# Performance work log

Hardware: AMD Instinct MI355X
Metric: run time of the kernel (lower is better)

Reference implementation:

```python
import jax, jax.numpy as jnp
import numpy as np

# geomloss SamplesLoss(loss='sinkhorn', p=2, reach=1.0, blur=0.1) constants
P = 2
BLUR = 0.1
REACH = 1.0
SCALING = 0.5
EPS_FINAL = BLUR ** P          # 0.01
RHO = REACH ** P               # 1.0
DIAMETER = 2.0 * np.sqrt(2.0)  # PMT positions scaled to [-1,1]^2


def eps_schedule():
    # geomloss epsilon_schedule(p, diameter, blur, scaling)
    e = [DIAMETER ** P]
    for t in np.arange(P * np.log(DIAMETER), P * np.log(BLUR), P * np.log(SCALING)):
        e.append(float(np.exp(t)))
    e.append(BLUR ** P)
    return [float(v) for v in e]


def _softmin(eps, C, h):
    # h: (B, N) log-measure + potential/eps ; C: (N, N) shared cost -> (B, N)
    return -eps * jax.scipy.special.logsumexp(h[:, None, :] - C[None, :, :] / eps, axis=-1)


def _sinkhorn_potentials(a_log, b_log, C):
    # symmetric unbalanced Sinkhorn loop with eps-annealing (geomloss sinkhorn_loop)
    eps_list = eps_schedule()
    damp = lambda eps: 1.0 / (1.0 + eps / RHO)
    eps0 = eps_list[0]
    d0 = damp(eps0)
    g_ab = d0 * _softmin(eps0, C, a_log)
    f_ba = d0 * _softmin(eps0, C, b_log)
    f_aa = d0 * _softmin(eps0, C, a_log)
    g_bb = d0 * _softmin(eps0, C, b_log)
    for eps in eps_list:
        d = damp(eps)
        ft = d * _softmin(eps, C, b_log + g_ab / eps)
        gt = d * _softmin(eps, C, a_log + f_ba / eps)
        f_ba, g_ab = 0.5 * (f_ba + ft), 0.5 * (g_ab + gt)
        f_aa = 0.5 * (f_aa + d * _softmin(eps, C, a_log + f_aa / eps))
        g_bb = 0.5 * (g_bb + d * _softmin(eps, C, b_log + g_bb / eps))
    # last extrapolation at the final (target) temperature
    eps = eps_list[-1]
    d = damp(eps)
    f_ba, g_ab = (d * _softmin(eps, C, b_log + g_ab / eps),
                  d * _softmin(eps, C, a_log + f_ba / eps))
    f_aa = d * _softmin(eps, C, a_log + f_aa / eps)
    g_bb = d * _softmin(eps, C, b_log + g_bb / eps)
    return f_aa, g_bb, g_ab, f_ba


def setup_inputs() -> dict:
    key = jax.random.key(0)
    k1, k2, k3 = jax.random.split(key, 3)
    B, N = 32768, 32
    # positive PE weights (measure masses must be > 0 for log-domain Sinkhorn)
    pred_pmtpe = jax.random.uniform(k1, (B, N), jnp.float32, 0.05, 1.0)
    target_pe = jax.random.uniform(k2, (B, N), jnp.float32, 0.05, 1.0)
    # fixed scaled 2D (z,y) PMT layout in [-1,1]^2, shared by pred and target clouds
    pmt_pos = jax.random.uniform(k3, (N, 2), jnp.float32, -1.0, 1.0)
    batchstart = jnp.arange(B, dtype=jnp.int64) * N
    batchend = batchstart + N
    return {"pred_pmtpe": pred_pmtpe, "target_pe": target_pe, "pmt_pos": pmt_pos,
            "batchstart": batchstart, "batchend": batchend}


def reference(pred_pmtpe, target_pe, pmt_pos, batchstart, batchend):
    # shared cost matrix (x_pred_batch == y_target_batch == PMT layout), C = |x-y|^2/2 for p=2
    C = 0.5 * jnp.sum((pmt_pos[:, None, :] - pmt_pos[None, :, :]) ** 2, axis=-1)  # (32,32)
    # geomloss runs the Sinkhorn loop with autograd disabled (envelope theorem)
    a_log = jnp.log(jax.lax.stop_gradient(pred_pmtpe))
    b_log = jnp.log(jax.lax.stop_gradient(target_pe))
    f_aa, g_bb, g_ab, f_ba = _sinkhorn_potentials(a_log, b_log, C)
    f_aa, g_bb, g_ab, f_ba = map(jax.lax.stop_gradient, (f_aa, g_bb, g_ab, f_ba))
    # unbalanced debiased sinkhorn cost (geomloss sinkhorn_cost, rho finite)
    eps = EPS_FINAL
    scale = RHO + 0.5 * eps
    per_batch = scale * (
        jnp.sum(pred_pmtpe * (jnp.exp(-f_aa / RHO) - jnp.exp(-f_ba / RHO)), axis=-1)
        + jnp.sum(target_pe * (jnp.exp(-g_bb / RHO) - jnp.exp(-g_ab / RHO)), axis=-1)
    )
    return jnp.mean(per_batch)
```

## Files before the change

kernel.cpp:

```cpp
#include <hip/hip_runtime.h>

#define EXP2F(x)  __builtin_amdgcn_exp2f(x)
#define LOG2FD(x) __builtin_amdgcn_logf(x)
#define L2E 1.4426950408889634f
#define T1F 1.2621774e-29f

typedef __attribute__((ext_vector_type(8))) short bf16x8;
typedef __attribute__((ext_vector_type(4))) float f32x4;

#define MFMA16(A, B, C) __builtin_amdgcn_mfma_f32_16x16x32_bf16((A), (B), (C), 0, 0, 0)

union U8 { unsigned int u[4]; bf16x8 v; };

__device__ __forceinline__ void split_pack(const float* w, bf16x8& hi, bf16x8& lo) {
  U8 a, b;
#pragma unroll
  for (int k = 0; k < 4; ++k) {
    float x0 = w[2*k], x1 = w[2*k+1];
    unsigned u0 = __float_as_uint(x0) & 0xFFFF0000u;
    unsigned u1 = __float_as_uint(x1) & 0xFFFF0000u;
    float r0 = x0 - __uint_as_float(u0);
    float r1 = x1 - __uint_as_float(u1);
    a.u[k] = (u0 >> 16) | u1;
    b.u[k] = ((__float_as_uint(r0) & 0xFFFF0000u) >> 16) |
             (__float_as_uint(r1) & 0xFFFF0000u);
  }
  hi = a.v; lo = b.v;
}

struct P1 {
  bf16x8 KA1, KA2, KB1, KB2;
  float Gab[8], Fba[8], Faa[8], Gbb[8];
  float al2[8], bl2[8];
};

__device__ __forceinline__ void buildK(const float* c2a, const float* c2b, float inv,
                                       bf16x8& KA1, bf16x8& KA2, bf16x8& KB1, bf16x8& KB2) {
  float ka[8], kb[8];
#pragma unroll
  for (int e = 0; e < 8; ++e) { ka[e] = EXP2F(-c2a[e] * inv); kb[e] = EXP2F(-c2b[e] * inv); }
  split_pack(ka, KA1, KA2);
  split_pack(kb, KB1, KB2);
}

__device__ __forceinline__ void pot_assign(float* pot, const float* Ts, int b15, int g) {
  float4 r0 = *(const float4*)&Ts[b15*36 + 8*g];
  float4 r1 = *(const float4*)&Ts[b15*36 + 8*g + 4];
  pot[0]=r0.x; pot[1]=r0.y; pot[2]=r0.z; pot[3]=r0.w;
  pot[4]=r1.x; pot[5]=r1.y; pot[6]=r1.z; pot[7]=r1.w;
}

__device__ __forceinline__ void pot_merge(float* pot, const float* Ts, int b15, int g) {
  float4 r0 = *(const float4*)&Ts[b15*36 + 8*g];
  float4 r1 = *(const float4*)&Ts[b15*36 + 8*g + 4];
  pot[0]=0.5f*(pot[0]+r0.x); pot[1]=0.5f*(pot[1]+r0.y);
  pot[2]=0.5f*(pot[2]+r0.z); pot[3]=0.5f*(pot[3]+r0.w);
  pot[4]=0.5f*(pot[4]+r1.x); pot[5]=0.5f*(pot[5]+r1.y);
  pot[6]=0.5f*(pot[6]+r1.z); pot[7]=0.5f*(pot[7]+r1.w);
}

__device__ __noinline__ float exact_lse(const float2* pos2, const float* HB,
                                        int i, float inv) {
  float2 pi = pos2[i];
  float m = -3.4e38f;
#pragma unroll 1
  for (int j = 0; j < 32; ++j) {
    float2 pj = pos2[j];
    float dx = pi.x - pj.x, dy = pi.y - pj.y;
    float arg = fmaf((0.5f*L2E)*(dx*dx + dy*dy), -inv, HB[j]);
    m = fmaxf(m, arg);
  }
  float s = 0.f;
#pragma unroll 1
  for (int j = 0; j < 32; ++j) {
    float2 pj = pos2[j];
    float dx = pi.x - pj.x, dy = pi.y - pj.y;
    float arg = fmaf((0.5f*L2E)*(dx*dx + dy*dy), -inv, HB[j]);
    s += EXP2F(arg - m);
  }
  return m + LOG2FD(s);
}

template<bool CHECKED>
__device__ __forceinline__ void ksoft(float* Ts, float* Hdump, const float* H,
    bf16x8 KA1, bf16x8 KA2, bf16x8 KB1, bf16x8 KB2,
    float nde, float inv, int b15, int g, const float2* pos2) {
  float hm = fmaxf(fmaxf(fmaxf(H[0], H[1]), fmaxf(H[2], H[3])),
                   fmaxf(fmaxf(H[4], H[5]), fmaxf(H[6], H[7])));
  hm = fmaxf(hm, __shfl_xor(hm, 16));
  hm = fmaxf(hm, __shfl_xor(hm, 32));
  float d[8], w[8];
#pragma unroll
  for (int e = 0; e < 8; ++e) { d[e] = H[e] - hm; w[e] = EXP2F(d[e]); }
  bf16x8 w1, w2;
  split_pack(w, w1, w2);
  f32x4 z = {0.f, 0.f, 0.f, 0.f};
  f32x4 a0 = MFMA16(KA1, w1, z);
  a0 = MFMA16(KA2, w1, a0);
  a0 = MFMA16(KA1, w2, a0);
  f32x4 a1 = MFMA16(KB1, w1, z);
  a1 = MFMA16(KB2, w1, a1);
  a1 = MFMA16(KB1, w2, a1);
  float r0[4], r1[4];
#pragma unroll
  for (int r = 0; r < 4; ++r) {
    r0[r] = hm + LOG2FD(a0[r]);
    r1[r] = hm + LOG2FD(a1[r]);
  }
  if (CHECKED) {
    float mn = fminf(fminf(fminf(a0[0], a0[1]), fminf(a0[2], a0[3])),
                     fminf(fminf(a1[0], a1[1]), fminf(a1[2], a1[3])));
    if (__any(mn < T1F)) {
      float wb[8];
#pragma unroll
      for (int e = 0; e < 8; ++e) wb[e] = EXP2F(d[e] + 96.f);
      bf16x8 u1, u2;
      split_pack(wb, u1, u2);
      f32x4 b0 = MFMA16(KA1, u1, z);
      b0 = MFMA16(KA2, u1, b0);
      b0 = MFMA16(KA1, u2, b0);
      f32x4 b1 = MFMA16(KB1, u1, z);
      b1 = MFMA16(KB2, u1, b1);
      b1 = MFMA16(KB1, u2, b1);
      bool mybad = false;
#pragma unroll
      for (int r = 0; r < 4; ++r) {
        if (a0[r] < T1F) r0[r] = (hm - 96.f) + LOG2FD(b0[r]);
        if (a1[r] < T1F) r1[r] = (hm - 96.f) + LOG2FD(b1[r]);
        mybad |= (a0[r] < T1F) && (b0[r] < T1F);
        mybad |= (a1[r] < T1F) && (b1[r] < T1F);
      }
      if (__any(mybad)) {
        float4 h0 = {H[0], H[1], H[2], H[3]};
        float4 h1 = {H[4], H[5], H[6], H[7]};
        *(float4*)&Hdump[b15*36 + 8*g]     = h0;
        *(float4*)&Hdump[b15*36 + 8*g + 4] = h1;
        asm volatile("" ::: "memory");
        const float* HB = &Hdump[b15*36];
#pragma unroll
        for (int r = 0; r < 4; ++r) {
          if ((a0[r] < T1F) && (b0[r] < T1F)) r0[r] = exact_lse(pos2, HB, 4*g + r, inv);
          if ((a1[r] < T1F) && (b1[r] < T1F)) r1[r] = exact_lse(pos2, HB, 16 + 4*g + r, inv);
        }
      }
    }
  }
  float4 v0 = {nde*r0[0], nde*r0[1], nde*r0[2], nde*r0[3]};
  float4 v1 = {nde*r1[0], nde*r1[1], nde*r1[2], nde*r1[3]};
  *(float4*)&Ts[b15*36 + 4*g]      = v0;
  *(float4*)&Ts[b15*36 + 4*g + 16] = v1;
}

template<bool CHECKED>
__device__ __forceinline__ void p_iter(P1& s, float* Tw, float* Hdump,
    float inv, float nde, bool mergeFirst, int b15, int g, const float2* pos2) {
  if (mergeFirst) {
    pot_merge(s.Fba, Tw + 0*576, b15, g);
    pot_merge(s.Gab, Tw + 1*576, b15, g);
    pot_merge(s.Faa, Tw + 2*576, b15, g);
    pot_merge(s.Gbb, Tw + 3*576, b15, g);
  }
  float H[8];
#pragma unroll
  for (int e = 0; e < 8; ++e) H[e] = fmaf(s.Gab[e], inv, s.bl2[e]);
  ksoft<CHECKED>(Tw + 0*576, Hdump, H, s.KA1, s.KA2, s.KB1, s.KB2, nde, inv, b15, g, pos2);
#pragma unroll
  for (int e = 0; e < 8; ++e) H[e] = fmaf(s.Fba[e], inv, s.al2[e]);
  ksoft<CHECKED>(Tw + 1*576, Hdump, H, s.KA1, s.KA2, s.KB1, s.KB2, nde, inv, b15, g, pos2);
#pragma unroll
  for (int e = 0; e < 8; ++e) H[e] = fmaf(s.Faa[e], inv, s.al2[e]);
  ksoft<CHECKED>(Tw + 2*576, Hdump, H, s.KA1, s.KA2, s.KB1, s.KB2, nde, inv, b15, g, pos2);
#pragma unroll
  for (int e = 0; e < 8; ++e) H[e] = fmaf(s.Gbb[e], inv, s.bl2[e]);
  ksoft<CHECKED>(Tw + 3*576, Hdump, H, s.KA1, s.KA2, s.KB1, s.KB2, nde, inv, b15, g, pos2);
}

__global__ __launch_bounds__(64, 2) void sink_kernel(
    const float* __restrict__ pred, const float* __restrict__ tgt,
    const float* __restrict__ pos, float* __restrict__ ws) {
  __shared__ __align__(16) float sT[4][576];
  __shared__ __align__(16) float sHb[16][36];

  const int lid = threadIdx.x;
  const int b15 = lid & 15;
  const int g   = lid >> 4;
  const int bbase = blockIdx.x * 16;
  const float2* pos2 = (const float2*)pos;
  float* Tw = &sT[0][0];
  float* Hd = &sHb[0][0];

  P1 s;
  {
    const float* pr = &pred[(bbase + b15) * 32 + 8 * g];
    const float* tr = &tgt [(bbase + b15) * 32 + 8 * g];
    float4 p0 = *(const float4*)&pr[0];
    float4 p1 = *(const float4*)&pr[4];
    float4 t0 = *(const float4*)&tr[0];
    float4 t1 = *(const float4*)&tr[4];
    s.al2[0]=LOG2FD(p0.x); s.al2[1]=LOG2FD(p0.y); s.al2[2]=LOG2FD(p0.z); s.al2[3]=LOG2FD(p0.w);
    s.al2[4]=LOG2FD(p1.x); s.al2[5]=LOG2FD(p1.y); s.al2[6]=LOG2FD(p1.z); s.al2[7]=LOG2FD(p1.w);
    s.bl2[0]=LOG2FD(t0.x); s.bl2[1]=LOG2FD(t0.y); s.bl2[2]=LOG2FD(t0.z); s.bl2[3]=LOG2FD(t0.w);
    s.bl2[4]=LOG2FD(t1.x); s.bl2[5]=LOG2FD(t1.y); s.bl2[6]=LOG2FD(t1.z); s.bl2[7]=LOG2FD(t1.w);
  }
  float c2a[8], c2b[8];
  {
    float2 pm0 = pos2[b15];
    float2 pm1 = pos2[b15 + 16];
#pragma unroll
    for (int e = 0; e < 8; ++e) {
      float2 pj = pos2[8*g + e];
      float dx0 = pm0.x - pj.x, dy0 = pm0.y - pj.y;
      float dx1 = pm1.x - pj.x, dy1 = pm1.y - pj.y;
      c2a[e] = (0.5f*L2E)*(dx0*dx0 + dy0*dy0);
      c2b[e] = (0.5f*L2E)*(dx1*dx1 + dy1*dy1);
    }
  }

  buildK(c2a, c2b, 0.125f, s.KA1, s.KA2, s.KB1, s.KB2);
  ksoft<false>(Tw + 1*576, Hd, s.al2, s.KA1, s.KA2, s.KB1, s.KB2, -8.f/9.f, 0.125f, b15, g, pos2);
  ksoft<false>(Tw + 0*576, Hd, s.bl2, s.KA1, s.KA2, s.KB1, s.KB2, -8.f/9.f, 0.125f, b15, g, pos2);
  pot_assign(s.Gab, Tw + 1*576, b15, g);
  pot_assign(s.Fba, Tw + 0*576, b15, g);
#pragma unroll
  for (int e = 0; e < 8; ++e) { s.Faa[e] = s.Gab[e]; s.Gbb[e] = s.Fba[e]; }

  p_iter<false>(s, Tw, Hd, 0.125f, -8.f/9.f, false, b15, g, pos2);
  p_iter<false>(s, Tw, Hd, 0.125f, -8.f/9.f, true,  b15, g, pos2);
  buildK(c2a, c2b, 0.5f, s.KA1, s.KA2, s.KB1, s.KB2);
  p_iter<false>(s, Tw, Hd, 0.5f, -2.f/3.f, true, b15, g, pos2);
  buildK(c2a, c2b, 2.f, s.KA1, s.KA2, s.KB1, s.KB2);
  p_iter<false>(s, Tw, Hd, 2.f, -1.f/3.f, true, b15, g, pos2);
  buildK(c2a, c2b, 8.f, s.KA1, s.KA2, s.KB1, s.KB2);
  p_iter<false>(s, Tw, Hd, 8.f, -1.f/9.f, true, b15, g, pos2);
  buildK(c2a, c2b, 32.f, s.KA1, s.KA2, s.KB1, s.KB2);
  p_iter<true>(s, Tw, Hd, 32.f, -1.f/33.f, true, b15, g, pos2);
  buildK(c2a, c2b, 100.f, s.KA1, s.KA2, s.KB1, s.KB2);
  p_iter<true>(s, Tw, Hd, 100.f, -1.f/101.f, true, b15, g, pos2);

  pot_merge(s.Fba, Tw + 0*576, b15, g);
  pot_merge(s.Gab, Tw + 1*576, b15, g);
  pot_merge(s.Faa, Tw + 2*576, b15, g);
  pot_merge(s.Gbb, Tw + 3*576, b15, g);
  {
    float H[8];
#pragma unroll
    for (int e = 0; e < 8; ++e) H[e] = fmaf(s.Gab[e], 100.f, s.bl2[e]);
    ksoft<true>(Tw + 0*576, Hd, H, s.KA1, s.KA2, s.KB1, s.KB2, -1.f/101.f, 100.f, b15, g, pos2);
#pragma unroll
    for (int e = 0; e < 8; ++e) H[e] = fmaf(s.Fba[e], 100.f, s.al2[e]);
    ksoft<true>(Tw + 1*576, Hd, H, s.KA1, s.KA2, s.KB1, s.KB2, -1.f/101.f, 100.f, b15, g, pos2);
#pragma unroll
    for (int e = 0; e < 8; ++e) H[e] = fmaf(s.Faa[e], 100.f, s.al2[e]);
    ksoft<true>(Tw + 2*576, Hd, H, s.KA1, s.KA2, s.KB1, s.KB2, -1.f/101.f, 100.f, b15, g, pos2);
#pragma unroll
    for (int e = 0; e < 8; ++e) H[e] = fmaf(s.Gbb[e], 100.f, s.bl2[e]);
    ksoft<true>(Tw + 3*576, Hd, H, s.KA1, s.KA2, s.KB1, s.KB2, -1.f/101.f, 100.f, b15, g, pos2);
  }
  pot_assign(s.Fba, Tw + 0*576, b15, g);
  pot_assign(s.Gab, Tw + 1*576, b15, g);
  pot_assign(s.Faa, Tw + 2*576, b15, g);
  pot_assign(s.Gbb, Tw + 3*576, b15, g);

  float c = 0.f;
#pragma unroll
  for (int e = 0; e < 8; ++e) {
    c += EXP2F(s.al2[e]) * (EXP2F(-s.Faa[e]) - EXP2F(-s.Fba[e]))
       + EXP2F(s.bl2[e]) * (EXP2F(-s.Gbb[e]) - EXP2F(-s.Gab[e]));
  }
  c += __shfl_xor(c, 1);
  c += __shfl_xor(c, 2);
  c += __shfl_xor(c, 4);
  c += __shfl_xor(c, 8);
  c += __shfl_xor(c, 16);
  c += __shfl_xor(c, 32);
  if (lid == 0) ws[blockIdx.x] = c;
}

__global__ __launch_bounds__(256) void reduce_kernel(
    const float* __restrict__ ws, float* __restrict__ out, int n, float scale) {
  float s = 0.f;
  for (int i = threadIdx.x; i < n; i += 256) s += ws[i];
  s += __shfl_xor(s, 32);
  s += __shfl_xor(s, 16);
  s += __shfl_xor(s, 8);
  s += __shfl_xor(s, 4);
  s += __shfl_xor(s, 2);
  s += __shfl_xor(s, 1);
  __shared__ float a[4];
  if ((threadIdx.x & 63) == 0) a[threadIdx.x >> 6] = s;
  __syncthreads();
  if (threadIdx.x == 0) out[0] = ((a[0] + a[1]) + (a[2] + a[3])) * scale;
}

extern "C" void kernel_launch(void* const* d_in, const int* in_sizes, int n_in,
                              void* d_out, int out_size, void* d_ws, size_t ws_size,
                              hipStream_t stream) {
  const float* pred = (const float*)d_in[0];
  const float* tgt  = (const float*)d_in[1];
  const float* pos  = (const float*)d_in[2];
  const int B = in_sizes[0] / 32;
  const int nblocks = B / 16;
  float* ws = (float*)d_ws;

  sink_kernel<<<nblocks, 64, 0, stream>>>(pred, tgt, pos, ws);
  reduce_kernel<<<1, 256, 0, stream>>>(ws, (float*)d_out, nblocks,
                                       1.005f / (float)B);
}
```

Before: 30.33 us.

## Split cross and self Sinkhorn chains across two wavefronts per block

Each block now runs two wavefronts. Wave 0 handles the cross potentials (f_ba, g_ab) and wave 1 handles the self potentials (f_aa, g_bb), so each wave runs two softmin calls per iteration instead of four. This roughly halves the serial dependency chain per wave and doubles the number of wavefronts in flight. In exchange it duplicates the K construction and log loads in both waves, adds __syncthreads per iteration, and writes twice as many partial sums for the reduction.

```diff
diff --git a/kernel.cpp b/kernel.cpp
--- a/kernel.cpp
+++ b/kernel.cpp
@@ -27,12 +27,6 @@
   }
   hi = a.v; lo = b.v;
 }
-
-struct P1 {
-  bf16x8 KA1, KA2, KB1, KB2;
-  float Gab[8], Fba[8], Faa[8], Gbb[8];
-  float al2[8], bl2[8];
-};
 
 __device__ __forceinline__ void buildK(const float* c2a, const float* c2b, float inv,
                                        bf16x8& KA1, bf16x8& KA2, bf16x8& KB1, bf16x8& KB2) {
@@ -152,44 +146,40 @@
 }
 
 template<bool CHECKED>
-__device__ __forceinline__ void p_iter(P1& s, float* Tw, float* Hdump,
-    float inv, float nde, bool mergeFirst, int b15, int g, const float2* pos2) {
-  if (mergeFirst) {
-    pot_merge(s.Fba, Tw + 0*576, b15, g);
-    pot_merge(s.Gab, Tw + 1*576, b15, g);
-    pot_merge(s.Faa, Tw + 2*576, b15, g);
-    pot_merge(s.Gbb, Tw + 3*576, b15, g);
-  }
-  float H[8];
-#pragma unroll
-  for (int e = 0; e < 8; ++e) H[e] = fmaf(s.Gab[e], inv, s.bl2[e]);
-  ksoft<CHECKED>(Tw + 0*576, Hdump, H, s.KA1, s.KA2, s.KB1, s.KB2, nde, inv, b15, g, pos2);
-#pragma unroll
-  for (int e = 0; e < 8; ++e) H[e] = fmaf(s.Fba[e], inv, s.al2[e]);
-  ksoft<CHECKED>(Tw + 1*576, Hdump, H, s.KA1, s.KA2, s.KB1, s.KB2, nde, inv, b15, g, pos2);
-#pragma unroll
-  for (int e = 0; e < 8; ++e) H[e] = fmaf(s.Faa[e], inv, s.al2[e]);
-  ksoft<CHECKED>(Tw + 2*576, Hdump, H, s.KA1, s.KA2, s.KB1, s.KB2, nde, inv, b15, g, pos2);
-#pragma unroll
-  for (int e = 0; e < 8; ++e) H[e] = fmaf(s.Gbb[e], inv, s.bl2[e]);
-  ksoft<CHECKED>(Tw + 3*576, Hdump, H, s.KA1, s.KA2, s.KB1, s.KB2, nde, inv, b15, g, pos2);
-}
-
-__global__ __launch_bounds__(64, 2) void sink_kernel(
+__device__ __forceinline__ void chain_iter(bool cross, float* X, float* Y,
+    const float* al2, const float* bl2, float* TX, float* TY, float* Hd,
+    bf16x8 KA1, bf16x8 KA2, bf16x8 KB1, bf16x8 KB2,
+    float inv, float nde, bool avg, int b15, int g, const float2* pos2) {
+  float HX[8], HY[8];
+#pragma unroll
+  for (int e = 0; e < 8; ++e) {
+    float xin = cross ? Y[e] : X[e];
+    float yin = cross ? X[e] : Y[e];
+    HX[e] = fmaf(xin, inv, bl2[e]);
+    HY[e] = fmaf(yin, inv, al2[e]);
+  }
+  ksoft<CHECKED>(TX, Hd, HX, KA1, KA2, KB1, KB2, nde, inv, b15, g, pos2);
+  ksoft<CHECKED>(TY, Hd, HY, KA1, KA2, KB1, KB2, nde, inv, b15, g, pos2);
+  __syncthreads();
+  if (avg) { pot_merge(X, TX, b15, g);  pot_merge(Y, TY, b15, g); }
+  else     { pot_assign(X, TX, b15, g); pot_assign(Y, TY, b15, g); }
+}
+
+__global__ __launch_bounds__(128, 4) void sink_kernel(
     const float* __restrict__ pred, const float* __restrict__ tgt,
     const float* __restrict__ pos, float* __restrict__ ws) {
-  __shared__ __align__(16) float sT[4][576];
-  __shared__ __align__(16) float sHb[16][36];
-
-  const int lid = threadIdx.x;
+  __shared__ __align__(16) float sT[2][2][576];
+  __shared__ __align__(16) float sHb[2][16][36];
+
+  const int lid = threadIdx.x & 63;
+  const int wid = threadIdx.x >> 6;
+  const bool cross = (wid == 0);
   const int b15 = lid & 15;
   const int g   = lid >> 4;
   const int bbase = blockIdx.x * 16;
   const float2* pos2 = (const float2*)pos;
-  float* Tw = &sT[0][0];
-  float* Hd = &sHb[0][0];
-
-  P1 s;
+
+  float al2[8], bl2[8];
   {
     const float* pr = &pred[(bbase + b15) * 32 + 8 * g];
     const float* tr = &tgt [(bbase + b15) * 32 + 8 * g];
@@ -197,10 +187,10 @@
     float4 p1 = *(const float4*)&pr[4];
     float4 t0 = *(const float4*)&tr[0];
     float4 t1 = *(const float4*)&tr[4];
-    s.al2[0]=LOG2FD(p0.x); s.al2[1]=LOG2FD(p0.y); s.al2[2]=LOG2FD(p0.z); s.al2[3]=LOG2FD(p0.w);
-    s.al2[4]=LOG2FD(p1.x); s.al2[5]=LOG2FD(p1.y); s.al2[6]=LOG2FD(p1.z); s.al2[7]=LOG2FD(p1.w);
-    s.bl2[0]=LOG2FD(t0.x); s.bl2[1]=LOG2FD(t0.y); s.bl2[2]=LOG2FD(t0.z); s.bl2[3]=LOG2FD(t0.w);
-    s.bl2[4]=LOG2FD(t1.x); s.bl2[5]=LOG2FD(t1.y); s.bl2[6]=LOG2FD(t1.z); s.bl2[7]=LOG2FD(t1.w);
+    al2[0]=LOG2FD(p0.x); al2[1]=LOG2FD(p0.y); al2[2]=LOG2FD(p0.z); al2[3]=LOG2FD(p0.w);
+    al2[4]=LOG2FD(p1.x); al2[5]=LOG2FD(p1.y); al2[6]=LOG2FD(p1.z); al2[7]=LOG2FD(p1.w);
+    bl2[0]=LOG2FD(t0.x); bl2[1]=LOG2FD(t0.y); bl2[2]=LOG2FD(t0.z); bl2[3]=LOG2FD(t0.w);
+    bl2[4]=LOG2FD(t1.x); bl2[5]=LOG2FD(t1.y); bl2[6]=LOG2FD(t1.z); bl2[7]=LOG2FD(t1.w);
   }
   float c2a[8], c2b[8];
   {
@@ -216,64 +206,59 @@
     }
   }
 
-  buildK(c2a, c2b, 0.125f, s.KA1, s.KA2, s.KB1, s.KB2);
-  ksoft<false>(Tw + 1*576, Hd, s.al2, s.KA1, s.KA2, s.KB1, s.KB2, -8.f/9.f, 0.125f, b15, g, pos2);
-  ksoft<false>(Tw + 0*576, Hd, s.bl2, s.KA1, s.KA2, s.KB1, s.KB2, -8.f/9.f, 0.125f, b15, g, pos2);
-  pot_assign(s.Gab, Tw + 1*576, b15, g);
-  pot_assign(s.Fba, Tw + 0*576, b15, g);
-#pragma unroll
-  for (int e = 0; e < 8; ++e) { s.Faa[e] = s.Gab[e]; s.Gbb[e] = s.Fba[e]; }
-
-  p_iter<false>(s, Tw, Hd, 0.125f, -8.f/9.f, false, b15, g, pos2);
-  p_iter<false>(s, Tw, Hd, 0.125f, -8.f/9.f, true,  b15, g, pos2);
-  buildK(c2a, c2b, 0.5f, s.KA1, s.KA2, s.KB1, s.KB2);
-  p_iter<false>(s, Tw, Hd, 0.5f, -2.f/3.f, true, b15, g, pos2);
-  buildK(c2a, c2b, 2.f, s.KA1, s.KA2, s.KB1, s.KB2);
-  p_iter<false>(s, Tw, Hd, 2.f, -1.f/3.f, true, b15, g, pos2);
-  buildK(c2a, c2b, 8.f, s.KA1, s.KA2, s.KB1, s.KB2);
-  p_iter<false>(s, Tw, Hd, 8.f, -1.f/9.f, true, b15, g, pos2);
-  buildK(c2a, c2b, 32.f, s.KA1, s.KA2, s.KB1, s.KB2);
-  p_iter<true>(s, Tw, Hd, 32.f, -1.f/33.f, true, b15, g, pos2);
-  buildK(c2a, c2b, 100.f, s.KA1, s.KA2, s.KB1, s.KB2);
-  p_iter<true>(s, Tw, Hd, 100.f, -1.f/101.f, true, b15, g, pos2);
-
-  pot_merge(s.Fba, Tw + 0*576, b15, g);
-  pot_merge(s.Gab, Tw + 1*576, b15, g);
-  pot_merge(s.Faa, Tw + 2*576, b15, g);
-  pot_merge(s.Gbb, Tw + 3*576, b15, g);
-  {
-    float H[8];
-#pragma unroll
-    for (int e = 0; e < 8; ++e) H[e] = fmaf(s.Gab[e], 100.f, s.bl2[e]);
-    ksoft<true>(Tw + 0*576, Hd, H, s.KA1, s.KA2, s.KB1, s.KB2, -1.f/101.f, 100.f, b15, g, pos2);
-#pragma unroll
-    for (int e = 0; e < 8; ++e) H[e] = fmaf(s.Fba[e], 100.f, s.al2[e]);
-    ksoft<true>(Tw + 1*576, Hd, H, s.KA1, s.KA2, s.KB1, s.KB2, -1.f/101.f, 100.f, b15, g, pos2);
-#pragma unroll
-    for (int e = 0; e < 8; ++e) H[e] = fmaf(s.Faa[e], 100.f, s.al2[e]);
-    ksoft<true>(Tw + 2*576, Hd, H, s.KA1, s.KA2, s.KB1, s.KB2, -1.f/101.f, 100.f, b15, g, pos2);
-#pragma unroll
-    for (int e = 0; e < 8; ++e) H[e] = fmaf(s.Gbb[e], 100.f, s.bl2[e]);
-    ksoft<true>(Tw + 3*576, Hd, H, s.KA1, s.KA2, s.KB1, s.KB2, -1.f/101.f, 100.f, b15, g, pos2);
-  }
-  pot_assign(s.Fba, Tw + 0*576, b15, g);
-  pot_assign(s.Gab, Tw + 1*576, b15, g);
-  pot_assign(s.Faa, Tw + 2*576, b15, g);
-  pot_assign(s.Gbb, Tw + 3*576, b15, g);
-
-  float c = 0.f;
+  float* TX = &sT[wid][0][0];
+  float* TY = &sT[wid][1][0];
+  float* Hd = &sHb[wid][0][0];
+
+  bf16x8 KA1, KA2, KB1, KB2;
+  float X[8], Y[8];
+
+  buildK(c2a, c2b, 0.125f, KA1, KA2, KB1, KB2);
+  ksoft<false>(TX, Hd, bl2, KA1, KA2, KB1, KB2, -8.f/9.f, 0.125f, b15, g, pos2);
+  ksoft<false>(TY, Hd, al2, KA1, KA2, KB1, KB2, -8.f/9.f, 0.125f, b15, g, pos2);
+  __syncthreads();
+  pot_assign(X, TX, b15, g);
+  pot_assign(Y, TY, b15, g);
+
+  chain_iter<false>(cross, X, Y, al2, bl2, TX, TY, Hd, KA1,KA2,KB1,KB2,
+                    0.125f, -8.f/9.f, true, b15, g, pos2);
+  chain_iter<false>(cross, X, Y, al2, bl2, TX, TY, Hd, KA1,KA2,KB1,KB2,
+                    0.125f, -8.f/9.f, true, b15, g, pos2);
+  buildK(c2a, c2b, 0.5f, KA1, KA2, KB1, KB2);
+  chain_iter<false>(cross, X, Y, al2, bl2, TX, TY, Hd, KA1,KA2,KB1,KB2,
+                    0.5f, -2.f/3.f, true, b15, g, pos2);
+  buildK(c2a, c2b, 2.f, KA1, KA2, KB1, KB2);
+  chain_iter<false>(cross, X, Y, al2, bl2, TX, TY, Hd, KA1,KA2,KB1,KB2,
+                    2.f, -1.f/3.f, true, b15, g, pos2);
+  buildK(c2a, c2b, 8.f, KA1, KA2, KB1, KB2);
+  chain_iter<false>(cross, X, Y, al2, bl2, TX, TY, Hd, KA1,KA2,KB1,KB2,
+                    8.f, -1.f/9.f, true, b15, g, pos2);
+  buildK(c2a, c2b, 32.f, KA1, KA2, KB1, KB2);
+  chain_iter<true>(cross, X, Y, al2, bl2, TX, TY, Hd, KA1,KA2,KB1,KB2,
+                   32.f, -1.f/33.f, true, b15, g, pos2);
+  buildK(c2a, c2b, 100.f, KA1, KA2, KB1, KB2);
+  chain_iter<true>(cross, X, Y, al2, bl2, TX, TY, Hd, KA1,KA2,KB1,KB2,
+                   100.f, -1.f/101.f, true, b15, g, pos2);
+  chain_iter<true>(cross, X, Y, al2, bl2, TX, TY, Hd, KA1,KA2,KB1,KB2,
+                   100.f, -1.f/101.f, false, b15, g, pos2);
+
+  float part = 0.f;
 #pragma unroll
   for (int e = 0; e < 8; ++e) {
-    c += EXP2F(s.al2[e]) * (EXP2F(-s.Faa[e]) - EXP2F(-s.Fba[e]))
-       + EXP2F(s.bl2[e]) * (EXP2F(-s.Gbb[e]) - EXP2F(-s.Gab[e]));
-  }
-  c += __shfl_xor(c, 1);
-  c += __shfl_xor(c, 2);
-  c += __shfl_xor(c, 4);
-  c += __shfl_xor(c, 8);
-  c += __shfl_xor(c, 16);
-  c += __shfl_xor(c, 32);
-  if (lid == 0) ws[blockIdx.x] = c;
+    float pv = EXP2F(al2[e]), tv = EXP2F(bl2[e]);
+    float u = cross ? pv : tv;
+    float v = cross ? tv : pv;
+    float term = u * EXP2F(-X[e]) + v * EXP2F(-Y[e]);
+    part += cross ? -term : term;
+  }
+
+  part += __shfl_xor(part, 1);
+  part += __shfl_xor(part, 2);
+  part += __shfl_xor(part, 4);
+  part += __shfl_xor(part, 8);
+  part += __shfl_xor(part, 16);
+  part += __shfl_xor(part, 32);
+  if (lid == 0) ws[blockIdx.x * 2 + wid] = part;
 }
 
 __global__ __launch_bounds__(256) void reduce_kernel(
@@ -302,7 +287,7 @@
   const int nblocks = B / 16;
   float* ws = (float*)d_ws;
 
-  sink_kernel<<<nblocks, 64, 0, stream>>>(pred, tgt, pos, ws);
-  reduce_kernel<<<1, 256, 0, stream>>>(ws, (float*)d_out, nblocks,
+  sink_kernel<<<nblocks, 128, 0, stream>>>(pred, tgt, pos, ws);
+  reduce_kernel<<<1, 256, 0, stream>>>(ws, (float*)d_out, 2 * nblocks,
                                        1.005f / (float)B);
 }
```

Result: slower. 35.14 us (+15.9%).

## Batch four softmin evaluations per iteration and interleave their MFMA chains

Applied to the files above, without the earlier changes.

Replaces the per-potential softmin routine with a multi-query version that computes max, exp and bf16 split for all four potentials first, then issues their MFMA accumulation chains interleaved so the dependent matrix ops overlap. The cross-lane max over 32 lanes now uses a permlane32 swap instead of a shuffle. The unrolled epsilon schedule becomes two non-unrolled loops with table-driven temperatures, which shrinks code size. The cost is higher register pressure from holding four sets of intermediates at two waves per SIMD.

```diff
diff --git a/kernel.cpp b/kernel.cpp
--- a/kernel.cpp
+++ b/kernel.cpp
@@ -7,6 +7,7 @@
 
 typedef __attribute__((ext_vector_type(8))) short bf16x8;
 typedef __attribute__((ext_vector_type(4))) float f32x4;
+typedef __attribute__((ext_vector_type(2))) unsigned int u32x2;
 
 #define MFMA16(A, B, C) __builtin_amdgcn_mfma_f32_16x16x32_bf16((A), (B), (C), 0, 0, 0)
 
@@ -28,11 +29,11 @@
   hi = a.v; lo = b.v;
 }
 
-struct P1 {
-  bf16x8 KA1, KA2, KB1, KB2;
-  float Gab[8], Fba[8], Faa[8], Gbb[8];
-  float al2[8], bl2[8];
-};
+__device__ __forceinline__ float pmax32(float v) {
+  u32x2 r = __builtin_amdgcn_permlane32_swap(__float_as_uint(v), __float_as_uint(v),
+                                             false, false);
+  return fmaxf(__uint_as_float(r.x), __uint_as_float(r.y));
+}
 
 __device__ __forceinline__ void buildK(const float* c2a, const float* c2b, float inv,
                                        bf16x8& KA1, bf16x8& KA2, bf16x8& KB1, bf16x8& KB2) {
@@ -81,98 +82,85 @@
   return m + LOG2FD(s);
 }
 
-template<bool CHECKED>
-__device__ __forceinline__ void ksoft(float* Ts, float* Hdump, const float* H,
-    bf16x8 KA1, bf16x8 KA2, bf16x8 KB1, bf16x8 KB2,
+template<int NQ, bool CHECKED>
+__device__ __forceinline__ void ksoft_multi(float* Ts, float* Hdump,
+    const float Hq[][8], bf16x8 KA1, bf16x8 KA2, bf16x8 KB1, bf16x8 KB2,
     float nde, float inv, int b15, int g, const float2* pos2) {
-  float hm = fmaxf(fmaxf(fmaxf(H[0], H[1]), fmaxf(H[2], H[3])),
-                   fmaxf(fmaxf(H[4], H[5]), fmaxf(H[6], H[7])));
-  hm = fmaxf(hm, __shfl_xor(hm, 16));
-  hm = fmaxf(hm, __shfl_xor(hm, 32));
-  float d[8], w[8];
-#pragma unroll
-  for (int e = 0; e < 8; ++e) { d[e] = H[e] - hm; w[e] = EXP2F(d[e]); }
-  bf16x8 w1, w2;
-  split_pack(w, w1, w2);
-  f32x4 z = {0.f, 0.f, 0.f, 0.f};
-  f32x4 a0 = MFMA16(KA1, w1, z);
-  a0 = MFMA16(KA2, w1, a0);
-  a0 = MFMA16(KA1, w2, a0);
-  f32x4 a1 = MFMA16(KB1, w1, z);
-  a1 = MFMA16(KB2, w1, a1);
-  a1 = MFMA16(KB1, w2, a1);
-  float r0[4], r1[4];
-#pragma unroll
-  for (int r = 0; r < 4; ++r) {
-    r0[r] = hm + LOG2FD(a0[r]);
-    r1[r] = hm + LOG2FD(a1[r]);
-  }
-  if (CHECKED) {
-    float mn = fminf(fminf(fminf(a0[0], a0[1]), fminf(a0[2], a0[3])),
-                     fminf(fminf(a1[0], a1[1]), fminf(a1[2], a1[3])));
-    if (__any(mn < T1F)) {
-      float wb[8];
-#pragma unroll
-      for (int e = 0; e < 8; ++e) wb[e] = EXP2F(d[e] + 96.f);
-      bf16x8 u1, u2;
-      split_pack(wb, u1, u2);
-      f32x4 b0 = MFMA16(KA1, u1, z);
-      b0 = MFMA16(KA2, u1, b0);
-      b0 = MFMA16(KA1, u2, b0);
-      f32x4 b1 = MFMA16(KB1, u1, z);
-      b1 = MFMA16(KB2, u1, b1);
-      b1 = MFMA16(KB1, u2, b1);
-      bool mybad = false;
-#pragma unroll
-      for (int r = 0; r < 4; ++r) {
-        if (a0[r] < T1F) r0[r] = (hm - 96.f) + LOG2FD(b0[r]);
-        if (a1[r] < T1F) r1[r] = (hm - 96.f) + LOG2FD(b1[r]);
-        mybad |= (a0[r] < T1F) && (b0[r] < T1F);
-        mybad |= (a1[r] < T1F) && (b1[r] < T1F);
-      }
-      if (__any(mybad)) {
-        float4 h0 = {H[0], H[1], H[2], H[3]};
-        float4 h1 = {H[4], H[5], H[6], H[7]};
-        *(float4*)&Hdump[b15*36 + 8*g]     = h0;
-        *(float4*)&Hdump[b15*36 + 8*g + 4] = h1;
-        asm volatile("" ::: "memory");
-        const float* HB = &Hdump[b15*36];
+  float hm[NQ], d[NQ][8];
+  bf16x8 w1[NQ], w2[NQ];
+#pragma unroll
+  for (int q = 0; q < NQ; ++q) {
+    const float* H = Hq[q];
+    float m = fmaxf(fmaxf(fmaxf(H[0], H[1]), fmaxf(H[2], H[3])),
+                    fmaxf(fmaxf(H[4], H[5]), fmaxf(H[6], H[7])));
+    m = fmaxf(m, __shfl_xor(m, 16));
+    m = pmax32(m);
+    hm[q] = m;
+    float w[8];
+#pragma unroll
+    for (int e = 0; e < 8; ++e) { d[q][e] = H[e] - m; w[e] = EXP2F(d[q][e]); }
+    split_pack(w, w1[q], w2[q]);
+  }
+  f32x4 a0[NQ], a1[NQ];
+  const f32x4 z = {0.f, 0.f, 0.f, 0.f};
+#pragma unroll
+  for (int q = 0; q < NQ; ++q) { a0[q] = MFMA16(KA1, w1[q], z);     a1[q] = MFMA16(KB1, w1[q], z); }
+#pragma unroll
+  for (int q = 0; q < NQ; ++q) { a0[q] = MFMA16(KA2, w1[q], a0[q]); a1[q] = MFMA16(KB2, w1[q], a1[q]); }
+#pragma unroll
+  for (int q = 0; q < NQ; ++q) { a0[q] = MFMA16(KA1, w2[q], a0[q]); a1[q] = MFMA16(KB1, w2[q], a1[q]); }
+#pragma unroll
+  for (int q = 0; q < NQ; ++q) {
+    float r0[4], r1[4];
+#pragma unroll
+    for (int r = 0; r < 4; ++r) {
+      r0[r] = hm[q] + LOG2FD(a0[q][r]);
+      r1[r] = hm[q] + LOG2FD(a1[q][r]);
+    }
+    if (CHECKED) {
+      float mn = fminf(fminf(fminf(a0[q][0], a0[q][1]), fminf(a0[q][2], a0[q][3])),
+                       fminf(fminf(a1[q][0], a1[q][1]), fminf(a1[q][2], a1[q][3])));
+      if (__any(mn < T1F)) {
+        float wb[8];
+#pragma unroll
+        for (int e = 0; e < 8; ++e) wb[e] = EXP2F(d[q][e] + 96.f);
+        bf16x8 u1, u2;
+        split_pack(wb, u1, u2);
+        f32x4 b0 = MFMA16(KA1, u1, z);
+        b0 = MFMA16(KA2, u1, b0);
+        b0 = MFMA16(KA1, u2, b0);
+        f32x4 b1 = MFMA16(KB1, u1, z);
+        b1 = MFMA16(KB2, u1, b1);
+        b1 = MFMA16(KB1, u2, b1);
+        bool mybad = false;
 #pragma unroll
         for (int r = 0; r < 4; ++r) {
-          if ((a0[r] < T1F) && (b0[r] < T1F)) r0[r] = exact_lse(pos2, HB, 4*g + r, inv);
-          if ((a1[r] < T1F) && (b1[r] < T1F)) r1[r] = exact_lse(pos2, HB, 16 + 4*g + r, inv);
+          if (a0[q][r] < T1F) r0[r] = (hm[q] - 96.f) + LOG2FD(b0[r]);
+          if (a1[q][r] < T1F) r1[r] = (hm[q] - 96.f) + LOG2FD(b1[r]);
+          mybad |= (a0[q][r] < T1F) && (b0[r] < T1F);
+          mybad |= (a1[q][r] < T1F) && (b1[r] < T1F);
+        }
+        if (__any(mybad)) {
+          float4 h0 = {Hq[q][0], Hq[q][1], Hq[q][2], Hq[q][3]};
+          float4 h1 = {Hq[q][4], Hq[q][5], Hq[q][6], Hq[q][7]};
+          *(float4*)&Hdump[b15*36 + 8*g]     = h0;
+          *(float4*)&Hdump[b15*36 + 8*g + 4] = h1;
+          asm volatile("" ::: "memory");
+          const float* HB = &Hdump[b15*36];
+#pragma unroll
+          for (int r = 0; r < 4; ++r) {
+            if ((a0[q][r] < T1F) && (b0[r] < T1F)) r0[r] = exact_lse(pos2, HB, 4*g + r, inv);
+            if ((a1[q][r] < T1F) && (b1[r] < T1F)) r1[r] = exact_lse(pos2, HB, 16 + 4*g + r, inv);
+          }
         }
       }
     }
-  }
-  float4 v0 = {nde*r0[0], nde*r0[1], nde*r0[2], nde*r0[3]};
-  float4 v1 = {nde*r1[0], nde*r1[1], nde*r1[2], nde*r1[3]};
-  *(float4*)&Ts[b15*36 + 4*g]      = v0;
-  *(float4*)&Ts[b15*36 + 4*g + 16] = v1;
-}
-
-template<bool CHECKED>
-__device__ __forceinline__ void p_iter(P1& s, float* Tw, float* Hdump,
-    float inv, float nde, bool mergeFirst, int b15, int g, const float2* pos2) {
-  if (mergeFirst) {
-    pot_merge(s.Fba, Tw + 0*576, b15, g);
-    pot_merge(s.Gab, Tw + 1*576, b15, g);
-    pot_merge(s.Faa, Tw + 2*576, b15, g);
-    pot_merge(s.Gbb, Tw + 3*576, b15, g);
-  }
-  float H[8];
-#pragma unroll
-  for (int e = 0; e < 8; ++e) H[e] = fmaf(s.Gab[e], inv, s.bl2[e]);
-  ksoft<CHECKED>(Tw + 0*576, Hdump, H, s.KA1, s.KA2, s.KB1, s.KB2, nde, inv, b15, g, pos2);
-#pragma unroll
-  for (int e = 0; e < 8; ++e) H[e] = fmaf(s.Fba[e], inv, s.al2[e]);
-  ksoft<CHECKED>(Tw + 1*576, Hdump, H, s.KA1, s.KA2, s.KB1, s.KB2, nde, inv, b15, g, pos2);
-#pragma unroll
-  for (int e = 0; e < 8; ++e) H[e] = fmaf(s.Faa[e], inv, s.al2[e]);
-  ksoft<CHECKED>(Tw + 2*576, Hdump, H, s.KA1, s.KA2, s.KB1, s.KB2, nde, inv, b15, g, pos2);
-#pragma unroll
-  for (int e = 0; e < 8; ++e) H[e] = fmaf(s.Gbb[e], inv, s.bl2[e]);
-  ksoft<CHECKED>(Tw + 3*576, Hdump, H, s.KA1, s.KA2, s.KB1, s.KB2, nde, inv, b15, g, pos2);
+    float4 v0 = {nde*r0[0], nde*r0[1], nde*r0[2], nde*r0[3]};
+    float4 v1 = {nde*r1[0], nde*r1[1], nde*r1[2], nde*r1[3]};
+    float* Tq = Ts + q * 576;
+    *(float4*)&Tq[b15*36 + 4*g]      = v0;
+    *(float4*)&Tq[b15*36 + 4*g + 16] = v1;
+  }
 }
 
 __global__ __launch_bounds__(64, 2) void sink_kernel(
@@ -189,7 +177,7 @@
   float* Tw = &sT[0][0];
   float* Hd = &sHb[0][0];
 
-  P1 s;
+  float al2[8], bl2[8];
   {
     const float* pr = &pred[(bbase + b15) * 32 + 8 * g];
     const float* tr = &tgt [(bbase + b15) * 32 + 8 * g];
@@ -197,10 +185,10 @@
     float4 p1 = *(const float4*)&pr[4];
     float4 t0 = *(const float4*)&tr[0];
     float4 t1 = *(const float4*)&tr[4];
-    s.al2[0]=LOG2FD(p0.x); s.al2[1]=LOG2FD(p0.y); s.al2[2]=LOG2FD(p0.z); s.al2[3]=LOG2FD(p0.w);
-    s.al2[4]=LOG2FD(p1.x); s.al2[5]=LOG2FD(p1.y); s.al2[6]=LOG2FD(p1.z); s.al2[7]=LOG2FD(p1.w);
-    s.bl2[0]=LOG2FD(t0.x); s.bl2[1]=LOG2FD(t0.y); s.bl2[2]=LOG2FD(t0.z); s.bl2[3]=LOG2FD(t0.w);
-    s.bl2[4]=LOG2FD(t1.x); s.bl2[5]=LOG2FD(t1.y); s.bl2[6]=LOG2FD(t1.z); s.bl2[7]=LOG2FD(t1.w);
+    al2[0]=LOG2FD(p0.x); al2[1]=LOG2FD(p0.y); al2[2]=LOG2FD(p0.z); al2[3]=LOG2FD(p0.w);
+    al2[4]=LOG2FD(p1.x); al2[5]=LOG2FD(p1.y); al2[6]=LOG2FD(p1.z); al2[7]=LOG2FD(p1.w);
+    bl2[0]=LOG2FD(t0.x); bl2[1]=LOG2FD(t0.y); bl2[2]=LOG2FD(t0.z); bl2[3]=LOG2FD(t0.w);
+    bl2[4]=LOG2FD(t1.x); bl2[5]=LOG2FD(t1.y); bl2[6]=LOG2FD(t1.z); bl2[7]=LOG2FD(t1.w);
   }
   float c2a[8], c2b[8];
   {
@@ -216,56 +204,77 @@
     }
   }
 
-  buildK(c2a, c2b, 0.125f, s.KA1, s.KA2, s.KB1, s.KB2);
-  ksoft<false>(Tw + 1*576, Hd, s.al2, s.KA1, s.KA2, s.KB1, s.KB2, -8.f/9.f, 0.125f, b15, g, pos2);
-  ksoft<false>(Tw + 0*576, Hd, s.bl2, s.KA1, s.KA2, s.KB1, s.KB2, -8.f/9.f, 0.125f, b15, g, pos2);
-  pot_assign(s.Gab, Tw + 1*576, b15, g);
-  pot_assign(s.Fba, Tw + 0*576, b15, g);
-#pragma unroll
-  for (int e = 0; e < 8; ++e) { s.Faa[e] = s.Gab[e]; s.Gbb[e] = s.Fba[e]; }
-
-  p_iter<false>(s, Tw, Hd, 0.125f, -8.f/9.f, false, b15, g, pos2);
-  p_iter<false>(s, Tw, Hd, 0.125f, -8.f/9.f, true,  b15, g, pos2);
-  buildK(c2a, c2b, 0.5f, s.KA1, s.KA2, s.KB1, s.KB2);
-  p_iter<false>(s, Tw, Hd, 0.5f, -2.f/3.f, true, b15, g, pos2);
-  buildK(c2a, c2b, 2.f, s.KA1, s.KA2, s.KB1, s.KB2);
-  p_iter<false>(s, Tw, Hd, 2.f, -1.f/3.f, true, b15, g, pos2);
-  buildK(c2a, c2b, 8.f, s.KA1, s.KA2, s.KB1, s.KB2);
-  p_iter<false>(s, Tw, Hd, 8.f, -1.f/9.f, true, b15, g, pos2);
-  buildK(c2a, c2b, 32.f, s.KA1, s.KA2, s.KB1, s.KB2);
-  p_iter<true>(s, Tw, Hd, 32.f, -1.f/33.f, true, b15, g, pos2);
-  buildK(c2a, c2b, 100.f, s.KA1, s.KA2, s.KB1, s.KB2);
-  p_iter<true>(s, Tw, Hd, 100.f, -1.f/101.f, true, b15, g, pos2);
-
-  pot_merge(s.Fba, Tw + 0*576, b15, g);
-  pot_merge(s.Gab, Tw + 1*576, b15, g);
-  pot_merge(s.Faa, Tw + 2*576, b15, g);
-  pot_merge(s.Gbb, Tw + 3*576, b15, g);
+  bf16x8 KA1, KA2, KB1, KB2;
+  float Fba[8], Gab[8], Faa[8], Gbb[8];
+
+  buildK(c2a, c2b, 0.125f, KA1, KA2, KB1, KB2);
   {
-    float H[8];
-#pragma unroll
-    for (int e = 0; e < 8; ++e) H[e] = fmaf(s.Gab[e], 100.f, s.bl2[e]);
-    ksoft<true>(Tw + 0*576, Hd, H, s.KA1, s.KA2, s.KB1, s.KB2, -1.f/101.f, 100.f, b15, g, pos2);
-#pragma unroll
-    for (int e = 0; e < 8; ++e) H[e] = fmaf(s.Fba[e], 100.f, s.al2[e]);
-    ksoft<true>(Tw + 1*576, Hd, H, s.KA1, s.KA2, s.KB1, s.KB2, -1.f/101.f, 100.f, b15, g, pos2);
-#pragma unroll
-    for (int e = 0; e < 8; ++e) H[e] = fmaf(s.Faa[e], 100.f, s.al2[e]);
-    ksoft<true>(Tw + 2*576, Hd, H, s.KA1, s.KA2, s.KB1, s.KB2, -1.f/101.f, 100.f, b15, g, pos2);
-#pragma unroll
-    for (int e = 0; e < 8; ++e) H[e] = fmaf(s.Gbb[e], 100.f, s.bl2[e]);
-    ksoft<true>(Tw + 3*576, Hd, H, s.KA1, s.KA2, s.KB1, s.KB2, -1.f/101.f, 100.f, b15, g, pos2);
-  }
-  pot_assign(s.Fba, Tw + 0*576, b15, g);
-  pot_assign(s.Gab, Tw + 1*576, b15, g);
-  pot_assign(s.Faa, Tw + 2*576, b15, g);
-  pot_assign(s.Gbb, Tw + 3*576, b15, g);
+    float Hq[2][8];
+#pragma unroll
+    for (int e = 0; e < 8; ++e) { Hq[0][e] = bl2[e]; Hq[1][e] = al2[e]; }
+    ksoft_multi<2, false>(Tw, Hd, Hq, KA1, KA2, KB1, KB2, -8.f/9.f, 0.125f, b15, g, pos2);
+  }
+  pot_assign(Fba, Tw + 0*576, b15, g);
+  pot_assign(Gab, Tw + 1*576, b15, g);
+#pragma unroll
+  for (int e = 0; e < 8; ++e) { Faa[e] = Gab[e]; Gbb[e] = Fba[e]; }
+
+  const float INV[8] = {0.125f, 0.125f, 0.5f, 2.f, 8.f, 32.f, 100.f, 100.f};
+  const float NDE[8] = {-8.f/9.f, -8.f/9.f, -2.f/3.f, -1.f/3.f, -1.f/9.f,
+                        -1.f/33.f, -1.f/101.f, -1.f/101.f};
+  float curInv = 0.125f;
+
+#pragma unroll 1
+  for (int k = 0; k < 5; ++k) {
+    const float inv = INV[k], nde = NDE[k];
+    if (inv != curInv) { buildK(c2a, c2b, inv, KA1, KA2, KB1, KB2); curInv = inv; }
+    float Hq[4][8];
+#pragma unroll
+    for (int e = 0; e < 8; ++e) {
+      Hq[0][e] = fmaf(Gab[e], inv, bl2[e]);
+      Hq[1][e] = fmaf(Fba[e], inv, al2[e]);
+      Hq[2][e] = fmaf(Faa[e], inv, al2[e]);
+      Hq[3][e] = fmaf(Gbb[e], inv, bl2[e]);
+    }
+    ksoft_multi<4, false>(Tw, Hd, Hq, KA1, KA2, KB1, KB2, nde, inv, b15, g, pos2);
+    pot_merge(Fba, Tw + 0*576, b15, g);
+    pot_merge(Gab, Tw + 1*576, b15, g);
+    pot_merge(Faa, Tw + 2*576, b15, g);
+    pot_merge(Gbb, Tw + 3*576, b15, g);
+  }
+
+#pragma unroll 1
+  for (int k = 5; k < 8; ++k) {
+    const float inv = INV[k], nde = NDE[k];
+    if (inv != curInv) { buildK(c2a, c2b, inv, KA1, KA2, KB1, KB2); curInv = inv; }
+    const bool avg = (k < 7);
+    float Hq[4][8];
+#pragma unroll
+    for (int e = 0; e < 8; ++e) {
+      Hq[0][e] = fmaf(Gab[e], inv, bl2[e]);
+      Hq[1][e] = fmaf(Fba[e], inv, al2[e]);
+      Hq[2][e] = fmaf(Faa[e], inv, al2[e]);
+      Hq[3][e] = fmaf(Gbb[e], inv, bl2[e]);
+    }
+    ksoft_multi<4, true>(Tw, Hd, Hq, KA1, KA2, KB1, KB2, nde, inv, b15, g, pos2);
+    if (avg) {
+      pot_merge(Fba, Tw + 0*576, b15, g);
+      pot_merge(Gab, Tw + 1*576, b15, g);
+      pot_merge(Faa, Tw + 2*576, b15, g);
+      pot_merge(Gbb, Tw + 3*576, b15, g);
+    } else {
+      pot_assign(Fba, Tw + 0*576, b15, g);
+      pot_assign(Gab, Tw + 1*576, b15, g);
+      pot_assign(Faa, Tw + 2*576, b15, g);
+      pot_assign(Gbb, Tw + 3*576, b15, g);
+    }
+  }
 
   float c = 0.f;
 #pragma unroll
   for (int e = 0; e < 8; ++e) {
-    c += EXP2F(s.al2[e]) * (EXP2F(-s.Faa[e]) - EXP2F(-s.Fba[e]))
-       + EXP2F(s.bl2[e]) * (EXP2F(-s.Gbb[e]) - EXP2F(-s.Gab[e]));
+    c += EXP2F(al2[e]) * (EXP2F(-Faa[e]) - EXP2F(-Fba[e]))
+       + EXP2F(bl2[e]) * (EXP2F(-Gbb[e]) - EXP2F(-Gab[e]));
   }
   c += __shfl_xor(c, 1);
   c += __shfl_xor(c, 2);
```

After: 28.97 us. -4.5%, faster.
